# Optimization experiments

Measured on AMD Instinct MI355X. Metric: run time of the kernel, lower is better.

The kernel has to match this reference:

```python
import jax, jax.numpy as jnp
import numpy as np
from jax import lax


def conv3x3(x, w):
    # x: [B, Cin, H, W], w: [Cout, Cin, 3, 3], padding=1, no bias
    return lax.conv_general_dilated(
        x, w, window_strides=(1, 1), padding=((1, 1), (1, 1)),
        dimension_numbers=("NCHW", "OIHW", "NCHW"))


def setup_inputs() -> dict:
    key = jax.random.key(0)
    k1, k2, k3, k4, k5 = jax.random.split(key, 5)
    N_NODES, N_EDGES, C, H, W = 4096, 32768, 32, 8, 8
    inp = jax.random.normal(k1, (N_NODES, C, H, W), dtype=jnp.float32)
    e = jax.random.normal(k2, (N_EDGES, C, H, W), dtype=jnp.float32)
    edge_sources = jax.random.randint(k3, (N_EDGES,), 0, N_NODES, dtype=jnp.int64) if jax.config.jax_enable_x64 else jax.random.randint(k3, (N_EDGES,), 0, N_NODES, dtype=jnp.int32)
    # conv weights, fan-in scaled
    scale = 1.0 / np.sqrt(C * 9)
    w_node = jax.random.normal(k4, (C, C, 3, 3), dtype=jnp.float32) * scale
    w_edge = jax.random.normal(k5, (C, C, 3, 3), dtype=jnp.float32) * scale
    return {"input": inp, "edge_sources": edge_sources, "e": e,
            "w_node": w_node, "w_edge": w_edge}


def reference(input, edge_sources, e, w_node, w_edge):
    # NOTE: node_linears has exactly one layer, so zip() runs a single iteration
    # even when n_layers > 1 (faithful to the original module).
    z = conv3x3(e, w_edge)                    # [E, Cout, H, W]
    th = conv3x3(input, w_node)[edge_sources]  # gather node conv output per edge
    z = jax.nn.elu(th * z)                    # net_type == 0 path
    return z
```

## Files before the change

### kernel.cpp

```cpp
#include <hip/hip_runtime.h>
#include <hip/hip_bf16.h>
#include <math.h>

typedef __attribute__((ext_vector_type(8))) short bf16x8;
typedef __attribute__((ext_vector_type(4))) float f32x4;

#define EPW 8
#define WAVES 4
#define XS 40
#define WST 296

__device__ __forceinline__ unsigned short bf16bits(float f) {
    union { __hip_bfloat16 h; unsigned short u; } cv;
    cv.h = __float2bfloat16(f);
    return cv.u;
}

__device__ __forceinline__ void stage_img(const float* __restrict__ g,
                                          unsigned short* xw, int lane) {
    #pragma unroll
    for (int i = 0; i < 16; ++i) {
        float v0 = g[(2 * i) * 64 + lane];
        float v1 = g[(2 * i + 1) * 64 + lane];
        unsigned int pk = (unsigned int)bf16bits(v0) |
                          ((unsigned int)bf16bits(v1) << 16);
        *(unsigned int*)&xw[lane * XS + 2 * i] = pk;
    }
}

__device__ __forceinline__ void conv_mfma(const unsigned short* __restrict__ xw,
                                          const unsigned short* __restrict__ wl,
                                          int m, int quad, f32x4 acc[2][4]) {
    #pragma unroll
    for (int kb = 0; kb < 9; ++kb) {
        const int kh = kb / 3, kw = kb - kh * 3;
        bf16x8 a0 = *(const bf16x8*)&wl[ m        * WST + kb * 32 + quad * 8];
        bf16x8 a1 = *(const bf16x8*)&wl[(m + 16)  * WST + kb * 32 + quad * 8];
        #pragma unroll
        for (int nt = 0; nt < 4; ++nt) {
            const int p  = nt * 16 + m;
            const int ih = (p >> 3) + kh - 1;
            const int iw = (p & 7) + kw - 1;
            const bool valid = ((unsigned)ih < 8u) && ((unsigned)iw < 8u);
            const int pixp = valid ? (ih * 8 + iw) : 0;
            bf16x8 b = *(const bf16x8*)&xw[pixp * XS + quad * 8];
            if (!valid) b = (bf16x8)(short)0;
            acc[0][nt] = __builtin_amdgcn_mfma_f32_16x16x32_bf16(a0, b, acc[0][nt], 0, 0, 0);
            acc[1][nt] = __builtin_amdgcn_mfma_f32_16x16x32_bf16(a1, b, acc[1][nt], 0, 0, 0);
        }
    }
}

__global__ __launch_bounds__(256, 2)
void fused_edge_kernel(const float* __restrict__ input,
                       const int* __restrict__ srcv,
                       const float* __restrict__ e,
                       const float* __restrict__ w_node,
                       const float* __restrict__ w_edge,
                       float* __restrict__ out,
                       int n_edges)
{
    __shared__ __align__(16) unsigned short w_lds[2][32 * WST];
    __shared__ __align__(16) unsigned short x_lds[WAVES][64 * XS];

    const int t = threadIdx.x;
    const int lane = t & 63;
    const int wave = t >> 6;

    for (int i = t; i < 9216; i += 256) {
        int co  = i / 288;
        int rem = i - co * 288;
        int ci  = rem / 9;
        int khw = rem - ci * 9;
        int dst = co * WST + khw * 32 + ci;
        w_lds[0][dst] = bf16bits(w_edge[i]);
        w_lds[1][dst] = bf16bits(w_node[i]);
    }
    __syncthreads();

    const int m    = lane & 15;
    const int quad = lane >> 4;
    unsigned short* xw = x_lds[wave];

    const int img0 = (blockIdx.x * WAVES + wave) * EPW;

    for (int j = 0; j < EPW; ++j) {
        const int img = img0 + j;
        if (img >= n_edges) break;

        f32x4 accz[2][4], acct[2][4];
        #pragma unroll
        for (int a = 0; a < 2; ++a)
            #pragma unroll
            for (int b = 0; b < 4; ++b) { accz[a][b] = (f32x4)0.f; acct[a][b] = (f32x4)0.f; }

        stage_img(e + (size_t)img * 2048, xw, lane);
        conv_mfma(xw, w_lds[0], m, quad, accz);

        stage_img(input + (size_t)srcv[img] * 2048, xw, lane);
        conv_mfma(xw, w_lds[1], m, quad, acct);

        float* op = out + (size_t)img * 2048;
        #pragma unroll
        for (int mt = 0; mt < 2; ++mt)
            #pragma unroll
            for (int nt = 0; nt < 4; ++nt)
                #pragma unroll
                for (int r = 0; r < 4; ++r) {
                    const int co = mt * 16 + quad * 4 + r;
                    const int p  = nt * 16 + m;
                    float v = accz[mt][nt][r] * acct[mt][nt][r];
                    op[co * 64 + p] = v > 0.f ? v : (__expf(v) - 1.f);
                }
    }
}

extern "C" void kernel_launch(void* const* d_in, const int* in_sizes, int n_in,
                              void* d_out, int out_size, void* d_ws, size_t ws_size,
                              hipStream_t stream)
{
    const float* input        = (const float*)d_in[0];
    const int*   edge_sources = (const int*)  d_in[1];
    const float* e            = (const float*)d_in[2];
    const float* w_node       = (const float*)d_in[3];
    const float* w_edge       = (const float*)d_in[4];
    float* out = (float*)d_out;
    (void)d_ws; (void)ws_size;

    const int n_edges = in_sizes[1];
    const int per_block = WAVES * EPW;
    const int grid = (n_edges + per_block - 1) / per_block;

    fused_edge_kernel<<<dim3(grid), dim3(256), 0, stream>>>(
        input, edge_sources, e, w_node, w_edge, out, n_edges);
}
```

Measured before the change: 499.8 us.

## Precompute node conv once per node, then gather in edge kernel with prefetch

Measured after the change: 666.9 us. 33.4% more time.

```diff
diff --git a/kernel.cpp b/kernel.cpp
--- a/kernel.cpp
+++ b/kernel.cpp
@@ -16,15 +16,28 @@
     return cv.u;
 }
 
-__device__ __forceinline__ void stage_img(const float* __restrict__ g,
-                                          unsigned short* xw, int lane) {
+__device__ __forceinline__ void load_img(const float* __restrict__ g, float* r, int lane) {
+    #pragma unroll
+    for (int i = 0; i < 32; ++i) r[i] = g[i * 64 + lane];
+}
+
+__device__ __forceinline__ void write_img(const float* r, unsigned short* xw, int lane) {
     #pragma unroll
     for (int i = 0; i < 16; ++i) {
-        float v0 = g[(2 * i) * 64 + lane];
-        float v1 = g[(2 * i + 1) * 64 + lane];
-        unsigned int pk = (unsigned int)bf16bits(v0) |
-                          ((unsigned int)bf16bits(v1) << 16);
+        unsigned int pk = (unsigned int)bf16bits(r[2 * i]) |
+                          ((unsigned int)bf16bits(r[2 * i + 1]) << 16);
         *(unsigned int*)&xw[lane * XS + 2 * i] = pk;
+    }
+}
+
+__device__ __forceinline__ void stage_weights(const float* __restrict__ w,
+                                              unsigned short* wl, int t) {
+    for (int i = t; i < 9216; i += 256) {
+        int co  = i / 288;
+        int rem = i - co * 288;
+        int ci  = rem / 9;
+        int khw = rem - ci * 9;
+        wl[co * WST + khw * 32 + ci] = bf16bits(w[i]);
     }
 }
 
@@ -51,6 +64,114 @@
     }
 }
 
+__global__ __launch_bounds__(256, 3)
+void node_conv_kernel(const float* __restrict__ input,
+                      const float* __restrict__ w_node,
+                      float* __restrict__ th, int n_nodes)
+{
+    __shared__ __align__(16) unsigned short w_lds[32 * WST];
+    __shared__ __align__(16) unsigned short x_lds[WAVES][64 * XS];
+
+    const int t = threadIdx.x, lane = t & 63, wave = t >> 6;
+    stage_weights(w_node, w_lds, t);
+    __syncthreads();
+
+    const int m = lane & 15, quad = lane >> 4;
+    unsigned short* xw = x_lds[wave];
+    const int n0 = (blockIdx.x * WAVES + wave) * EPW;
+
+    float ereg[32];
+    if (n0 < n_nodes) load_img(input + (size_t)n0 * 2048, ereg, lane);
+
+    for (int j = 0; j < EPW; ++j) {
+        const int nd = n0 + j;
+        if (nd >= n_nodes) break;
+
+        write_img(ereg, xw, lane);
+        if (j + 1 < EPW && nd + 1 < n_nodes)
+            load_img(input + (size_t)(nd + 1) * 2048, ereg, lane);
+
+        f32x4 acc[2][4];
+        #pragma unroll
+        for (int a = 0; a < 2; ++a)
+            #pragma unroll
+            for (int b = 0; b < 4; ++b) acc[a][b] = (f32x4)0.f;
+
+        conv_mfma(xw, w_lds, m, quad, acc);
+
+        float* op = th + (size_t)nd * 2048;
+        #pragma unroll
+        for (int mt = 0; mt < 2; ++mt)
+            #pragma unroll
+            for (int nt = 0; nt < 4; ++nt) {
+                const int p = nt * 16 + m;
+                *(f32x4*)&op[p * 32 + mt * 16 + quad * 4] = acc[mt][nt];
+            }
+    }
+}
+
+__global__ __launch_bounds__(256, 3)
+void edge_mul_kernel(const float* __restrict__ e,
+                     const int* __restrict__ srcv,
+                     const float* __restrict__ th,
+                     const float* __restrict__ w_edge,
+                     float* __restrict__ out, int n_edges)
+{
+    __shared__ __align__(16) unsigned short w_lds[32 * WST];
+    __shared__ __align__(16) unsigned short x_lds[WAVES][64 * XS];
+
+    const int t = threadIdx.x, lane = t & 63, wave = t >> 6;
+    stage_weights(w_edge, w_lds, t);
+    __syncthreads();
+
+    const int m = lane & 15, quad = lane >> 4;
+    unsigned short* xw = x_lds[wave];
+    const int img0 = (blockIdx.x * WAVES + wave) * EPW;
+
+    float ereg[32];
+    if (img0 < n_edges) load_img(e + (size_t)img0 * 2048, ereg, lane);
+
+    for (int j = 0; j < EPW; ++j) {
+        const int img = img0 + j;
+        if (img >= n_edges) break;
+
+        write_img(ereg, xw, lane);
+
+        const int src = srcv[img];
+        const float* tp = th + (size_t)src * 2048;
+        f32x4 T[2][4];
+        #pragma unroll
+        for (int mt = 0; mt < 2; ++mt)
+            #pragma unroll
+            for (int nt = 0; nt < 4; ++nt)
+                T[mt][nt] = *(const f32x4*)&tp[(nt * 16 + m) * 32 + mt * 16 + quad * 4];
+
+        if (j + 1 < EPW && img + 1 < n_edges)
+            load_img(e + (size_t)(img + 1) * 2048, ereg, lane);
+
+        f32x4 acc[2][4];
+        #pragma unroll
+        for (int a = 0; a < 2; ++a)
+            #pragma unroll
+            for (int b = 0; b < 4; ++b) acc[a][b] = (f32x4)0.f;
+
+        conv_mfma(xw, w_lds, m, quad, acc);
+
+        float* op = out + (size_t)img * 2048;
+        #pragma unroll
+        for (int mt = 0; mt < 2; ++mt)
+            #pragma unroll
+            for (int nt = 0; nt < 4; ++nt)
+                #pragma unroll
+                for (int r = 0; r < 4; ++r) {
+                    const int co = mt * 16 + quad * 4 + r;
+                    const int p  = nt * 16 + m;
+                    float v = T[mt][nt][r] * acc[mt][nt][r];
+                    op[co * 64 + p] = v > 0.f ? v : (__expf(v) - 1.f);
+                }
+    }
+}
+
 __global__ __launch_bounds__(256, 2)
 void fused_edge_kernel(const float* __restrict__ input,
                        const int* __restrict__ srcv,
@@ -94,10 +215,13 @@
             #pragma unroll
             for (int b = 0; b < 4; ++b) { accz[a][b] = (f32x4)0.f; acct[a][b] = (f32x4)0.f; }
 
-        stage_img(e + (size_t)img * 2048, xw, lane);
+        float ereg[32];
+        load_img(e + (size_t)img * 2048, ereg, lane);
+        write_img(ereg, xw, lane);
         conv_mfma(xw, w_lds[0], m, quad, accz);
 
-        stage_img(input + (size_t)srcv[img] * 2048, xw, lane);
+        load_img(input + (size_t)srcv[img] * 2048, ereg, lane);
+        write_img(ereg, xw, lane);
         conv_mfma(xw, w_lds[1], m, quad, acct);
 
         float* op = out + (size_t)img * 2048;
@@ -125,12 +249,23 @@
     const float* w_node       = (const float*)d_in[3];
     const float* w_edge       = (const float*)d_in[4];
     float* out = (float*)d_out;
-    (void)d_ws; (void)ws_size;
 
     const int n_edges = in_sizes[1];
+    const int n_nodes = in_sizes[0] > 65536 ? in_sizes[0] / 2048 : in_sizes[0];
+
     const int per_block = WAVES * EPW;
-    const int grid = (n_edges + per_block - 1) / per_block;
-
-    fused_edge_kernel<<<dim3(grid), dim3(256), 0, stream>>>(
-        input, edge_sources, e, w_node, w_edge, out, n_edges);
-}
+    const int egrid = (n_edges + per_block - 1) / per_block;
+
+    const size_t th_bytes = (size_t)n_nodes * 2048 * sizeof(float);
+
+    if (d_ws != nullptr && ws_size >= th_bytes) {
+        float* th = (float*)d_ws;
+        const int ngrid = (n_nodes + per_block - 1) / per_block;
+        node_conv_kernel<<<dim3(ngrid), dim3(256), 0, stream>>>(input, w_node, th, n_nodes);
+        edge_mul_kernel<<<dim3(egrid), dim3(256), 0, stream>>>(e, edge_sources, th, w_edge,
+                                                               out, n_edges);
+    } else {
+        fused_edge_kernel<<<dim3(egrid), dim3(256), 0, stream>>>(
+            input, edge_sources, e, w_node, w_edge, out, n_edges);
+    }
+}
```

## Prefetch next images into registers and widen blocks to eight waves

Applied to the files above, without the earlier changes.

Measured after the change: 839.2 us. 1.68x slower.

```diff
diff --git a/kernel.cpp b/kernel.cpp
--- a/kernel.cpp
+++ b/kernel.cpp
@@ -6,8 +6,8 @@
 typedef __attribute__((ext_vector_type(4))) float f32x4;
 
 #define EPW 8
-#define WAVES 4
 #define XS 40
+#define XROWS 65
 #define WST 296
 
 __device__ __forceinline__ unsigned short bf16bits(float f) {
@@ -16,14 +16,16 @@
     return cv.u;
 }
 
-__device__ __forceinline__ void stage_img(const float* __restrict__ g,
-                                          unsigned short* xw, int lane) {
+__device__ __forceinline__ void load_img(const float* __restrict__ g, float* r, int lane) {
+    #pragma unroll
+    for (int i = 0; i < 32; ++i) r[i] = g[i * 64 + lane];
+}
+
+__device__ __forceinline__ void write_img(const float* r, unsigned short* xw, int lane) {
     #pragma unroll
     for (int i = 0; i < 16; ++i) {
-        float v0 = g[(2 * i) * 64 + lane];
-        float v1 = g[(2 * i + 1) * 64 + lane];
-        unsigned int pk = (unsigned int)bf16bits(v0) |
-                          ((unsigned int)bf16bits(v1) << 16);
+        unsigned int pk = (unsigned int)bf16bits(r[2 * i]) |
+                          ((unsigned int)bf16bits(r[2 * i + 1]) << 16);
         *(unsigned int*)&xw[lane * XS + 2 * i] = pk;
     }
 }
@@ -42,16 +44,16 @@
             const int ih = (p >> 3) + kh - 1;
             const int iw = (p & 7) + kw - 1;
             const bool valid = ((unsigned)ih < 8u) && ((unsigned)iw < 8u);
-            const int pixp = valid ? (ih * 8 + iw) : 0;
+            const int pixp = valid ? (ih * 8 + iw) : 64;
             bf16x8 b = *(const bf16x8*)&xw[pixp * XS + quad * 8];
-            if (!valid) b = (bf16x8)(short)0;
             acc[0][nt] = __builtin_amdgcn_mfma_f32_16x16x32_bf16(a0, b, acc[0][nt], 0, 0, 0);
             acc[1][nt] = __builtin_amdgcn_mfma_f32_16x16x32_bf16(a1, b, acc[1][nt], 0, 0, 0);
         }
     }
 }
 
-__global__ __launch_bounds__(256, 2)
+template<int WAVES_T>
+__global__ __launch_bounds__(WAVES_T * 64, 4)
 void fused_edge_kernel(const float* __restrict__ input,
                        const int* __restrict__ srcv,
                        const float* __restrict__ e,
@@ -60,29 +62,38 @@
                        float* __restrict__ out,
                        int n_edges)
 {
-    __shared__ __align__(16) unsigned short w_lds[2][32 * WST];
-    __shared__ __align__(16) unsigned short x_lds[WAVES][64 * XS];
+    extern __shared__ unsigned short smem_u16[];
+    unsigned short* wl0 = smem_u16;
+    unsigned short* wl1 = smem_u16 + 32 * WST;
 
     const int t = threadIdx.x;
     const int lane = t & 63;
     const int wave = t >> 6;
+    unsigned short* xw = smem_u16 + 2 * 32 * WST + wave * (XROWS * XS);
 
-    for (int i = t; i < 9216; i += 256) {
+    for (int i = t; i < 9216; i += WAVES_T * 64) {
         int co  = i / 288;
         int rem = i - co * 288;
         int ci  = rem / 9;
         int khw = rem - ci * 9;
         int dst = co * WST + khw * 32 + ci;
-        w_lds[0][dst] = bf16bits(w_edge[i]);
-        w_lds[1][dst] = bf16bits(w_node[i]);
+        wl0[dst] = bf16bits(w_edge[i]);
+        wl1[dst] = bf16bits(w_node[i]);
     }
+    if (lane < XS) xw[64 * XS + lane] = 0;
     __syncthreads();
 
     const int m    = lane & 15;
     const int quad = lane >> 4;
-    unsigned short* xw = x_lds[wave];
 
-    const int img0 = (blockIdx.x * WAVES + wave) * EPW;
+    const int img0 = (blockIdx.x * WAVES_T + wave) * EPW;
+
+    float ereg[32];
+    int src = 0;
+    if (img0 < n_edges) {
+        load_img(e + (size_t)img0 * 2048, ereg, lane);
+        src = srcv[img0];
+    }
 
     for (int j = 0; j < EPW; ++j) {
         const int img = img0 + j;
@@ -94,11 +105,16 @@
             #pragma unroll
             for (int b = 0; b < 4; ++b) { accz[a][b] = (f32x4)0.f; acct[a][b] = (f32x4)0.f; }
 
-        stage_img(e + (size_t)img * 2048, xw, lane);
-        conv_mfma(xw, w_lds[0], m, quad, accz);
+        write_img(ereg, xw, lane);
+        float ireg[32];
+        load_img(input + (size_t)src * 2048, ireg, lane);
+        if (j + 1 < EPW && img + 1 < n_edges) src = srcv[img + 1];
+        conv_mfma(xw, wl0, m, quad, accz);
 
-        stage_img(input + (size_t)srcv[img] * 2048, xw, lane);
-        conv_mfma(xw, w_lds[1], m, quad, acct);
+        write_img(ireg, xw, lane);
+        if (j + 1 < EPW && img + 1 < n_edges)
+            load_img(e + (size_t)(img + 1) * 2048, ereg, lane);
+        conv_mfma(xw, wl1, m, quad, acct);
 
         float* op = out + (size_t)img * 2048;
         #pragma unroll
@@ -128,9 +144,27 @@
     (void)d_ws; (void)ws_size;
 
     const int n_edges = in_sizes[1];
-    const int per_block = WAVES * EPW;
-    const int grid = (n_edges + per_block - 1) / per_block;
 
-    fused_edge_kernel<<<dim3(grid), dim3(256), 0, stream>>>(
-        input, edge_sources, e, w_node, w_edge, out, n_edges);
+    const size_t lds8 = (size_t)(2 * 32 * WST + 8 * XROWS * XS) * sizeof(unsigned short);
+    const size_t lds4 = (size_t)(2 * 32 * WST + 4 * XROWS * XS) * sizeof(unsigned short);
+
+    static int use8 = -1;
+    if (use8 < 0) {
+        hipError_t err = hipFuncSetAttribute(
+            reinterpret_cast<const void*>(&fused_edge_kernel<8>),
+            hipFuncAttributeMaxDynamicSharedMemorySize, (int)lds8);
+        use8 = (err == hipSuccess) ? 1 : 0;
+    }
+
+    if (use8) {
+        const int per_block = 8 * EPW;
+        const int grid = (n_edges + per_block - 1) / per_block;
+        fused_edge_kernel<8><<<dim3(grid), dim3(512), lds8, stream>>>(
+            input, edge_sources, e, w_node, w_edge, out, n_edges);
+    } else {
+        const int per_block = 4 * EPW;
+        const int grid = (n_edges + per_block - 1) / per_block;
+        fused_edge_kernel<4><<<dim3(grid), dim3(256), lds4, stream>>>(
+            input, edge_sources, e, w_node, w_edge, out, n_edges);
+    }
 }
```
